# Performance work log

Measured on AMD Instinct MI355X. Metric: run time of the kernel, lower is better.

Reference implementation:

```python
import jax, jax.numpy as jnp
import numpy as np

EDGES_1B = [[1,2],[1,39],[2,3],[2,25],[3,4],[3,18],[4,5],[4,14],[5,6],[5,8],[6,7],[6,11],[7,8],[8,9],[9,39],[10,11],[10,13],[11,12],[13,14],[14,15],[15,16],[16,17],[16,19],[16,24],[17,18],[17,27],[19,20],[19,33],[20,21],[20,34],[21,22],[22,23],[22,35],[23,24],[23,36],[25,26],[25,37],[26,27],[26,28],[26,29],[28,29],[29,38],[30,38],[31,32],[33,34],[35,36]]
NUM_GRAPHS = 8192
NODES_PER_GRAPH = 39
HIDDEN = 128
NODE_F, EDGE_F, OUT_F = 4, 2, 2
EPS = 1e-5


def _build_edge_index():
    e0 = np.array([[u - 1, v - 1] for u, v in EDGES_1B], dtype=np.int64)
    e = np.concatenate([e0, e0[:, ::-1]], axis=0).T  # [2, 92] bidirectional
    off = np.arange(NUM_GRAPHS, dtype=np.int64) * NODES_PER_GRAPH
    ei = (e[:, None, :] + off[None, :, None]).reshape(2, -1)  # [2, 8192*92]
    return jnp.asarray(ei)


def setup_inputs() -> dict:
    key = jax.random.key(0)
    ks = jax.random.split(key, 16)
    N = NUM_GRAPHS * NODES_PER_GRAPH
    E = NUM_GRAPHS * 92

    def lin(k, fi, fo):
        k1, k2 = jax.random.split(k)
        s = 1.0 / np.sqrt(fi)
        return (jax.random.uniform(k1, (fi, fo), jnp.float32, -s, s),
                jax.random.uniform(k2, (fo,), jnp.float32, -s, s))

    W1a, b1a = lin(ks[0], 2 * NODE_F + EDGE_F, HIDDEN)
    W1b, b1b = lin(ks[1], HIDDEN, HIDDEN)
    W2a, b2a = lin(ks[2], 2 * HIDDEN + EDGE_F, HIDDEN)
    W2b, b2b = lin(ks[3], HIDDEN, HIDDEN)
    Wo, bo = lin(ks[4], HIDDEN, OUT_F)
    return {
        'x': jax.random.normal(ks[5], (N, NODE_F), jnp.float32),
        'edge_index': _build_edge_index(),
        'edge_attr': jax.random.normal(ks[6], (E, EDGE_F), jnp.float32),
        'W1a': W1a, 'b1a': b1a, 'W1b': W1b, 'b1b': b1b,
        'g1': jnp.ones((HIDDEN,), jnp.float32), 'be1': jnp.zeros((HIDDEN,), jnp.float32),
        'W2a': W2a, 'b2a': b2a, 'W2b': W2b, 'b2b': b2b,
        'g2': jnp.ones((HIDDEN,), jnp.float32), 'be2': jnp.zeros((HIDDEN,), jnp.float32),
        'Wo': Wo, 'bo': bo,
    }


def _gnn_layer(x, src, dst, edge_attr, Wa, ba, Wb, bb):
    # message: mlp(cat[x_i, x_j, edge_attr]) with x_i = target, x_j = source
    m = jnp.concatenate([x[dst], x[src], edge_attr], axis=1)  # [E, 2F+Fe]
    m = jax.nn.relu(m @ Wa + ba) @ Wb + bb                    # [E, H]
    N = x.shape[0]
    agg = jax.ops.segment_sum(m, dst, num_segments=N)         # scatter-sum
    cnt = jax.ops.segment_sum(jnp.ones((m.shape[0],), m.dtype), dst, num_segments=N)
    return agg / jnp.maximum(cnt, 1.0)[:, None]               # mean aggregation


def _batch_norm(x, gamma, beta):
    mu = jnp.mean(x, axis=0)
    var = jnp.mean(jnp.square(x - mu), axis=0)  # biased var (training-mode BN)
    return (x - mu) * jax.lax.rsqrt(var + EPS) * gamma + beta


def reference(x, edge_index, edge_attr, W1a, b1a, W1b, b1b, g1, be1,
              W2a, b2a, W2b, b2b, g2, be2, Wo, bo):
    src, dst = edge_index[0], edge_index[1]
    h = _gnn_layer(x, src, dst, edge_attr, W1a, b1a, W1b, b1b)
    h = jax.nn.relu(_batch_norm(h, g1, be1))
    h = _gnn_layer(h, src, dst, edge_attr, W2a, b2a, W2b, b2b)
    h = jax.nn.relu(_batch_norm(h, g2, be2))
    return h @ Wo + bo
```

## Files before the change

### kernel.cpp

```cpp
#include <hip/hip_runtime.h>
#include <hip/hip_bf16.h>

#define NG 8192
#define NPG 39
#define H 128
#define NTOT (NG*NPG)
#define INV_N (1.0f/319488.0f)
#define SHS 136

typedef __attribute__((ext_vector_type(8))) short bf16x8;
typedef __attribute__((ext_vector_type(4))) float f32x4;
typedef unsigned short u16;

__device__ __forceinline__ float u16tof(u16 u) {
  union { unsigned int i; float f; } v; v.i = ((unsigned int)u) << 16; return v.f;
}
__device__ __forceinline__ u16 ftou16(float f) {
  union { float f; unsigned int i; } v; v.f = f;
  const unsigned int x = v.i;
  return (u16)((x + 0x7FFFu + ((x >> 16) & 1u)) >> 16);
}

__constant__ int INC_OFF[40] = {0,2,5,8,11,14,17,19,22,24,26,29,30,32,35,37,41,44,46,49,
                                52,54,57,60,62,65,69,71,73,76,77,78,79,81,83,85,87,88,90,92};
__constant__ int INC_EID[92] = {
 46,47, 0,48,49, 2,50,51, 4,52,53, 6,54,55, 8,56,57, 10,58, 9,12,59, 13,60,
 61,62, 11,15,63, 17, 16,64, 7,18,65, 19,66, 20,67,68,69, 21,70,71, 5,24,
 22,72,73, 26,74,75, 28,76, 30,77,78, 31,79,80, 23,33, 3,81,82, 35,83,84,85,
 25,37, 38,86, 39,40,87, 88, 89, 43, 27,90, 29,44, 32,91, 34,45, 36, 41,42, 1,14};
__constant__ int INC_SRC[92] = {
 1,38, 0,2,24, 1,3,17, 2,4,13, 3,5,7, 4,6,10, 5,7, 4,6,8, 7,38,
 10,12, 5,9,11, 10, 9,13, 3,12,14, 13,15, 14,16,18,23, 15,17,26, 2,16,
 15,19,32, 18,20,33, 19,21, 20,22,34, 21,23,35, 15,22, 1,25,36, 24,26,27,28,
 16,25, 25,28, 25,27,37, 37, 31, 30, 18,33, 19,32, 21,35, 22,34, 24, 28,29, 0,8};
__constant__ float DEGINV[39] = {
 0.5f, 1.f/3, 1.f/3, 1.f/3, 1.f/3, 1.f/3, 0.5f, 1.f/3, 0.5f, 0.5f,
 1.f/3, 1.f,   0.5f, 1.f/3, 0.5f, 0.25f, 1.f/3, 0.5f, 1.f/3, 1.f/3,
 0.5f, 1.f/3, 1.f/3, 0.5f, 1.f/3, 0.25f, 0.5f, 0.5f, 1.f/3, 1.f,
 1.f,  1.f,   0.5f, 0.5f, 0.5f, 0.5f, 1.f,  0.5f, 0.5f};

__global__ __launch_bounds__(256)
void k_tr(const float* __restrict__ W2a, const float* __restrict__ W2b,
          const float* __restrict__ W1b, u16* __restrict__ WT)
{
  const int idx = blockIdx.x * 256 + threadIdx.x;
  const int mat = idx >> 14, rem = idx & 16383;
  const int n = rem >> 7, k = rem & 127;
  float v;
  if (mat == 0)      v = W2a[k*H + n];
  else if (mat == 1) v = W2a[(128 + k)*H + n];
  else if (mat == 2) v = W2b[k*H + n];
  else               v = W1b[k*H + n];
  WT[mat*16384 + n*128 + k] = ftou16(v);
}

__global__ __launch_bounds__(512, 8)
void k_layer1(const float* __restrict__ x, const float* __restrict__ ea,
              const float* __restrict__ W1a, const float* __restrict__ b1a,
              const u16* __restrict__ W1bT, const float* __restrict__ b1b,
              u16* __restrict__ h1, float* __restrict__ pstats)
{
  __shared__ alignas(16) u16 shb[48*SHS];
  __shared__ alignas(16) float sx[160];
  __shared__ alignas(16) float sea[184];
  const int g = blockIdx.x, tid = threadIdx.x;
  const int lane = tid & 63, wv = tid >> 6;
  const int qd = lane >> 4, ln = lane & 15;
  const int col = wv*16 + ln;

  for (int i = tid; i < 156; i += 512) sx[i] = x[g*156 + i];
  for (int i = tid; i < 184; i += 512) sea[i] = ea[g*184 + i];
  __syncthreads();

  {
    const int j = tid & 127;
    float wa[10];
    #pragma unroll
    for (int r = 0; r < 10; ++r) wa[r] = W1a[r*H + j];
    const float ba = b1a[j];
    for (int n = (tid >> 7); n < 39; n += 4) {
      const float4 xd = *(const float4*)&sx[n*4];
      const float xdot = ba + xd.x*wa[0] + xd.y*wa[1] + xd.z*wa[2] + xd.w*wa[3];
      float acc = 0.f;
      const int o1 = INC_OFF[n+1];
      for (int t = INC_OFF[n]; t < o1; ++t) {
        const int e = INC_EID[t], s = INC_SRC[t];
        const float4 xs = *(const float4*)&sx[s*4];
        const float2 se = *(const float2*)&sea[e*2];
        const float hv = xdot + xs.x*wa[4] + xs.y*wa[5] + xs.z*wa[6] + xs.w*wa[7]
                              + se.x*wa[8] + se.y*wa[9];
        acc += fmaxf(hv, 0.f);
      }
      shb[n*SHS + j] = ftou16(acc * DEGINV[n]);
    }
  }
  __syncthreads();

  {
    bf16x8 bw[4];
    const u16* wbp = W1bT + col*128 + qd*8;
    #pragma unroll
    for (int kt = 0; kt < 4; ++kt) bw[kt] = *(const bf16x8*)(wbp + kt*32);
    const float bcol = b1b[col];
    float ssum = 0.f, ssq = 0.f;
    #pragma unroll
    for (int mt = 0; mt < 3; ++mt) {
      bf16x8 a[4];
      const u16* ap = shb + (mt*16 + ln)*SHS + qd*8;
      #pragma unroll
      for (int kt = 0; kt < 4; ++kt) a[kt] = *(const bf16x8*)(ap + kt*32);
      f32x4 acc = {0.f,0.f,0.f,0.f};
      #pragma unroll
      for (int kt = 0; kt < 4; ++kt)
        acc = __builtin_amdgcn_mfma_f32_16x16x32_bf16(a[kt], bw[kt], acc, 0, 0, 0);
      #pragma unroll
      for (int r = 0; r < 4; ++r) {
        const int rw = mt*16 + qd*4 + r;
        if (rw < 39) {
          const float v = acc[r] + bcol;
          h1[(size_t)(g*39 + rw)*H + col] = ftou16(v);
          ssum += v; ssq += v*v;
        }
      }
    }
    ssum += __shfl_down(ssum, 32); ssum += __shfl_down(ssum, 16);
    ssq  += __shfl_down(ssq, 32);  ssq  += __shfl_down(ssq, 16);
    if (lane < 16) {
      pstats[(size_t)0*NG*H + (size_t)g*H + wv*16 + lane] = ssum;
      pstats[(size_t)1*NG*H + (size_t)g*H + wv*16 + lane] = ssq;
    }
  }
}

__global__ __launch_bounds__(256)
void k_red1(const float* __restrict__ pstats, float* __restrict__ part2)
{
  const int b = blockIdx.x, tid = threadIdx.x;
  const int j = tid & 127, p = tid >> 7;
  const float* base = pstats + (size_t)p*NG*H + (size_t)b*64*H + j;
  float s = 0.f;
  for (int r = 0; r < 64; ++r) s += base[r*H];
  part2[p*128*H + b*H + j] = s;
}

__global__ __launch_bounds__(256)
void k_red2(const float* __restrict__ part2, const float* __restrict__ gamma,
            const float* __restrict__ beta, float* __restrict__ sc)
{
  __shared__ float st[256];
  const int tid = threadIdx.x;
  const int j = tid & 127, p = tid >> 7;
  const float* base = part2 + p*128*H + j;
  float s = 0.f;
  for (int b = 0; b < 128; ++b) s += base[b*H];
  st[p*128 + j] = s;
  __syncthreads();
  if (tid < 128) {
    const float mu  = st[tid] * INV_N;
    const float var = st[128 + tid] * INV_N - mu*mu;
    const float inv = rsqrtf(fmaxf(var, 0.f) + 1e-5f);
    const float s1  = gamma[tid] * inv;
    sc[tid]       = s1;
    sc[128 + tid] = beta[tid] - mu * s1;
  }
}

__global__ __launch_bounds__(512, 8)
void k_layer2(const u16* __restrict__ h1, const float* __restrict__ ea,
              const float* __restrict__ sc1,
              const u16* __restrict__ WdT, const u16* __restrict__ WsT,
              const u16* __restrict__ WbT,
              const float* __restrict__ W2a, const float* __restrict__ b2a,
              const float* __restrict__ b2b,
              u16* __restrict__ h2, float* __restrict__ pstats)
{
  __shared__ alignas(16) u16 shb[48*SHS];
  __shared__ alignas(16) u16 pdb[48*SHS];
  __shared__ alignas(16) u16 psb[48*SHS];
  __shared__ alignas(16) float sea[184];
  const int g = blockIdx.x, tid = threadIdx.x;
  const int lane = tid & 63, wv = tid >> 6;
  const int qd = lane >> 4, ln = lane & 15;
  const int col = wv*16 + ln;

  for (int i = tid; i < 184; i += 512) sea[i] = ea[g*184 + i];
  {
    const u16* hp = h1 + (size_t)g*39*H;
    for (int i = tid; i < 1248; i += 512) {
      const int n = i >> 5, j = (i & 31) * 4;
      const ushort4 hv = ((const ushort4*)hp)[i];
      const float4 s0 = *(const float4*)&sc1[j];
      const float4 s1 = *(const float4*)&sc1[128 + j];
      ushort4 st;
      st.x = ftou16(fmaxf(u16tof(hv.x)*s0.x + s1.x, 0.f));
      st.y = ftou16(fmaxf(u16tof(hv.y)*s0.y + s1.y, 0.f));
      st.z = ftou16(fmaxf(u16tof(hv.z)*s0.z + s1.z, 0.f));
      st.w = ftou16(fmaxf(u16tof(hv.w)*s0.w + s1.w, 0.f));
      *(ushort4*)&shb[n*SHS + j] = st;
    }
  }
  __syncthreads();

  {
    bf16x8 bd[4], bs[4];
    const u16* wdp = WdT + col*128 + qd*8;
    const u16* wsp = WsT + col*128 + qd*8;
    #pragma unroll
    for (int kt = 0; kt < 4; ++kt) {
      bd[kt] = *(const bf16x8*)(wdp + kt*32);
      bs[kt] = *(const bf16x8*)(wsp + kt*32);
    }
    #pragma unroll
    for (int mt = 0; mt < 3; ++mt) {
      bf16x8 a[4];
      const u16* ap = shb + (mt*16 + ln)*SHS + qd*8;
      #pragma unroll
      for (int kt = 0; kt < 4; ++kt) a[kt] = *(const bf16x8*)(ap + kt*32);
      f32x4 accd = {0.f,0.f,0.f,0.f}, accs = {0.f,0.f,0.f,0.f};
      #pragma unroll
      for (int kt = 0; kt < 4; ++kt) {
        accd = __builtin_amdgcn_mfma_f32_16x16x32_bf16(a[kt], bd[kt], accd, 0, 0, 0);
        accs = __builtin_amdgcn_mfma_f32_16x16x32_bf16(a[kt], bs[kt], accs, 0, 0, 0);
      }
      #pragma unroll
      for (int r = 0; r < 4; ++r) {
        const int rw = mt*16 + qd*4 + r;
        pdb[rw*SHS + col] = ftou16(accd[r]);
        psb[rw*SHS + col] = ftou16(accs[r]);
      }
    }
  }
  __syncthreads();

  {
    const int j2 = tid & 63;
    const int nq = tid >> 6;
    const float2 w8 = *(const float2*)&W2a[256*H + 2*j2];
    const float2 w9 = *(const float2*)&W2a[257*H + 2*j2];
    const float2 b2 = *(const float2*)&b2a[2*j2];
    for (int n = nq; n < 39; n += 8) {
      const ushort2 pdu = *(const ushort2*)&pdb[n*SHS + 2*j2];
      const float base0 = u16tof(pdu.x) + b2.x;
      const float base1 = u16tof(pdu.y) + b2.y;
      float a0 = 0.f, a1 = 0.f;
      const int o1 = INC_OFF[n+1];
      for (int t = INC_OFF[n]; t < o1; ++t) {
        const int e = INC_EID[t], s = INC_SRC[t];
        const float2 se = *(const float2*)&sea[e*2];
        const ushort2 ps = *(const ushort2*)&psb[s*SHS + 2*j2];
        const float h0 = base0 + u16tof(ps.x) + se.x*w8.x + se.y*w9.x;
        const float h1v = base1 + u16tof(ps.y) + se.x*w8.y + se.y*w9.y;
        a0 += fmaxf(h0, 0.f);
        a1 += fmaxf(h1v, 0.f);
      }
      ushort2 st;
      st.x = ftou16(a0 * DEGINV[n]);
      st.y = ftou16(a1 * DEGINV[n]);
      *(ushort2*)&shb[n*SHS + 2*j2] = st;
    }
  }
  __syncthreads();

  {
    bf16x8 bb[4];
    const u16* wbp = WbT + col*128 + qd*8;
    #pragma unroll
    for (int kt = 0; kt < 4; ++kt) bb[kt] = *(const bf16x8*)(wbp + kt*32);
    const float bcol = b2b[col];
    float ssum = 0.f, ssq = 0.f;
    #pragma unroll
    for (int mt = 0; mt < 3; ++mt) {
      bf16x8 a[4];
      const u16* ap = shb + (mt*16 + ln)*SHS + qd*8;
      #pragma unroll
      for (int kt = 0; kt < 4; ++kt) a[kt] = *(const bf16x8*)(ap + kt*32);
      f32x4 acc = {0.f,0.f,0.f,0.f};
      #pragma unroll
      for (int kt = 0; kt < 4; ++kt)
        acc = __builtin_amdgcn_mfma_f32_16x16x32_bf16(a[kt], bb[kt], acc, 0, 0, 0);
      #pragma unroll
      for (int r = 0; r < 4; ++r) {
        const int rw = mt*16 + qd*4 + r;
        if (rw < 39) {
          const float v = acc[r] + bcol;
          h2[(size_t)(g*39 + rw)*H + col] = ftou16(v);
          ssum += v; ssq += v*v;
        }
      }
    }
    ssum += __shfl_down(ssum, 32); ssum += __shfl_down(ssum, 16);
    ssq  += __shfl_down(ssq, 32);  ssq  += __shfl_down(ssq, 16);
    if (lane < 16) {
      pstats[(size_t)0*NG*H + (size_t)g*H + wv*16 + lane] = ssum;
      pstats[(size_t)1*NG*H + (size_t)g*H + wv*16 + lane] = ssq;
    }
  }
}

__global__ __launch_bounds__(256)
void k_out(const u16* __restrict__ h2, const float* __restrict__ sc2,
           const float* __restrict__ Wo, const float* __restrict__ bo,
           float* __restrict__ out)
{
  const int tid = threadIdx.x;
  const int lane = tid & 63;
  const size_t n = (size_t)blockIdx.x*4 + (tid >> 6);
  const int c0 = lane, c1 = lane + 64;
  const float v0 = fmaxf(u16tof(h2[n*H + c0]) * sc2[c0] + sc2[128 + c0], 0.f);
  const float v1 = fmaxf(u16tof(h2[n*H + c1]) * sc2[c1] + sc2[128 + c1], 0.f);
  float a0 = v0*Wo[c0*2]   + v1*Wo[c1*2];
  float a1 = v0*Wo[c0*2+1] + v1*Wo[c1*2+1];
  #pragma unroll
  for (int off = 32; off > 0; off >>= 1) {
    a0 += __shfl_down(a0, off);
    a1 += __shfl_down(a1, off);
  }
  if (lane == 0) {
    *(float2*)&out[n*2] = make_float2(a0 + bo[0], a1 + bo[1]);
  }
}

extern "C" void kernel_launch(void* const* d_in, const int* in_sizes, int n_in,
                              void* d_out, int out_size, void* d_ws, size_t ws_size,
                              hipStream_t stream)
{
  const float* x   = (const float*)d_in[0];
  const float* ea  = (const float*)d_in[2];
  const float* W1a = (const float*)d_in[3];
  const float* b1a = (const float*)d_in[4];
  const float* W1b = (const float*)d_in[5];
  const float* b1b = (const float*)d_in[6];
  const float* g1  = (const float*)d_in[7];
  const float* be1 = (const float*)d_in[8];
  const float* W2a = (const float*)d_in[9];
  const float* b2a = (const float*)d_in[10];
  const float* W2b = (const float*)d_in[11];
  const float* b2b = (const float*)d_in[12];
  const float* g2  = (const float*)d_in[13];
  const float* be2 = (const float*)d_in[14];
  const float* Wo  = (const float*)d_in[15];
  const float* bo  = (const float*)d_in[16];
  float* out = (float*)d_out;

  char* ws = (char*)d_ws;
  size_t off = 0;
  u16* h1 = (u16*)(ws + off); off += (size_t)NTOT*H*2;
  u16* h2 = (u16*)(ws + off); off += (size_t)NTOT*H*2;
  float* pstats1 = (float*)(ws + off); off += (size_t)2*NG*H*4;
  float* pstats2 = (float*)(ws + off); off += (size_t)2*NG*H*4;
  float* p2a = (float*)(ws + off); off += (size_t)2*128*H*4;
  float* p2b = (float*)(ws + off); off += (size_t)2*128*H*4;
  float* sc1 = (float*)(ws + off); off += 256*4;
  float* sc2 = (float*)(ws + off); off += 256*4;
  u16* WT = (u16*)(ws + off); off += (size_t)4*16384*2;
  u16* WdT  = WT;
  u16* WsT  = WT + 16384;
  u16* WbT  = WT + 32768;
  u16* W1bT = WT + 49152;

  k_tr<<<256, 256, 0, stream>>>(W2a, W2b, W1b, WT);
  k_layer1<<<NG, 512, 0, stream>>>(x, ea, W1a, b1a, W1bT, b1b, h1, pstats1);
  k_red1<<<128, 256, 0, stream>>>(pstats1, p2a);
  k_red2<<<1, 256, 0, stream>>>(p2a, g1, be1, sc1);
  k_layer2<<<NG, 512, 0, stream>>>(h1, ea, sc1, WdT, WsT, WbT, W2a, b2a, b2b, h2, pstats2);
  k_red1<<<128, 256, 0, stream>>>(pstats2, p2b);
  k_red2<<<1, 256, 0, stream>>>(p2b, g2, be2, sc2);
  k_out<<<NTOT/4, 256, 0, stream>>>(h2, sc2, Wo, bo, out);
}
```

Measured before the change: 433.4 us.

## Compute layer-1 first edge MLP with bf16 MFMA over per-edge feature tiles

Layer 1's first linear layer was computed with scalar FMAs per (node, incident edge, hidden column). It now builds a padded bf16 edge-feature matrix [92 x 32] in shared memory, multiplies it by a pre-transposed bf16 W1a with one MFMA per 16-row tile, stores the ReLU'd messages in a new shared buffer, and then mean-aggregates them per node. This trades scalar ALU work for matrix-core work, but adds about 25 KB of shared memory per block, which may lower occupancy, and rounds the first-layer inputs and weights to bf16.

New measurement: 408.7 us. 5.7% less time.

```diff
diff --git a/kernel.cpp b/kernel.cpp
--- a/kernel.cpp
+++ b/kernel.cpp
@@ -7,8 +7,10 @@
 #define NTOT (NG*NPG)
 #define INV_N (1.0f/319488.0f)
 #define SHS 136
+#define ES 40
 
 typedef __attribute__((ext_vector_type(8))) short bf16x8;
+typedef __attribute__((ext_vector_type(8))) unsigned short u16x8;
 typedef __attribute__((ext_vector_type(4))) float f32x4;
 typedef unsigned short u16;
 
@@ -33,6 +35,12 @@
  10,12, 5,9,11, 10, 9,13, 3,12,14, 13,15, 14,16,18,23, 15,17,26, 2,16,
  15,19,32, 18,20,33, 19,21, 20,22,34, 21,23,35, 15,22, 1,25,36, 24,26,27,28,
  16,25, 25,28, 25,27,37, 37, 31, 30, 18,33, 19,32, 21,35, 22,34, 24, 28,29, 0,8};
+__constant__ int EDST[92] = {
+ 1,38,2,24,3,17,4,13,5,7,6,10,7,8,38,10,12,11,13,14,15,16,18,23,17,26,19,32,20,33,21,22,34,23,35,25,36,26,27,28,28,37,37,31,33,35,
+ 0,0,1,1,2,2,3,3,4,4,5,5,6,7,8,9,9,10,12,13,14,15,15,15,16,16,18,18,19,19,20,21,21,22,22,24,24,25,25,25,27,28,29,30,32,34};
+__constant__ int ESRC[92] = {
+ 0,0,1,1,2,2,3,3,4,4,5,5,6,7,8,9,9,10,12,13,14,15,15,15,16,16,18,18,19,19,20,21,21,22,22,24,24,25,25,25,27,28,29,30,32,34,
+ 1,38,2,24,3,17,4,13,5,7,6,10,7,8,38,10,12,11,13,14,15,16,18,23,17,26,19,32,20,33,21,22,34,23,35,25,36,26,27,28,28,37,37,31,33,35};
 __constant__ float DEGINV[39] = {
  0.5f, 1.f/3, 1.f/3, 1.f/3, 1.f/3, 1.f/3, 0.5f, 1.f/3, 0.5f, 0.5f,
  1.f/3, 1.f,   0.5f, 1.f/3, 0.5f, 0.25f, 1.f/3, 0.5f, 1.f/3, 1.f/3,
@@ -41,28 +49,38 @@
 
 __global__ __launch_bounds__(256)
 void k_tr(const float* __restrict__ W2a, const float* __restrict__ W2b,
-          const float* __restrict__ W1b, u16* __restrict__ WT)
+          const float* __restrict__ W1b, const float* __restrict__ W1a,
+          u16* __restrict__ WT)
 {
   const int idx = blockIdx.x * 256 + threadIdx.x;
-  const int mat = idx >> 14, rem = idx & 16383;
-  const int n = rem >> 7, k = rem & 127;
-  float v;
-  if (mat == 0)      v = W2a[k*H + n];
-  else if (mat == 1) v = W2a[(128 + k)*H + n];
-  else if (mat == 2) v = W2b[k*H + n];
-  else               v = W1b[k*H + n];
-  WT[mat*16384 + n*128 + k] = ftou16(v);
+  if (idx < 65536) {
+    const int mat = idx >> 14, rem = idx & 16383;
+    const int n = rem >> 7, k = rem & 127;
+    float v;
+    if (mat == 0)      v = W2a[k*H + n];
+    else if (mat == 1) v = W2a[(128 + k)*H + n];
+    else if (mat == 2) v = W2b[k*H + n];
+    else               v = W1b[k*H + n];
+    WT[mat*16384 + n*128 + k] = ftou16(v);
+  } else if (idx < 69632) {
+    const int rem = idx - 65536;
+    const int col = rem >> 5, k = rem & 31;
+    const float v = (k < 10) ? W1a[k*H + col] : 0.f;
+    WT[65536 + col*32 + k] = ftou16(v);
+  }
 }
 
 __global__ __launch_bounds__(512, 8)
 void k_layer1(const float* __restrict__ x, const float* __restrict__ ea,
-              const float* __restrict__ W1a, const float* __restrict__ b1a,
+              const u16* __restrict__ W1aT, const float* __restrict__ b1a,
               const u16* __restrict__ W1bT, const float* __restrict__ b1b,
               u16* __restrict__ h1, float* __restrict__ pstats)
 {
   __shared__ alignas(16) u16 shb[48*SHS];
+  __shared__ alignas(16) u16 msgb[92*SHS];
   __shared__ alignas(16) float sx[160];
   __shared__ alignas(16) float sea[184];
+  u16* Eb = shb;
   const int g = blockIdx.x, tid = threadIdx.x;
   const int lane = tid & 63, wv = tid >> 6;
   const int qd = lane >> 4, ln = lane & 15;
@@ -72,26 +90,58 @@
   for (int i = tid; i < 184; i += 512) sea[i] = ea[g*184 + i];
   __syncthreads();
 
-  {
-    const int j = tid & 127;
-    float wa[10];
-    #pragma unroll
-    for (int r = 0; r < 10; ++r) wa[r] = W1a[r*H + j];
-    const float ba = b1a[j];
-    for (int n = (tid >> 7); n < 39; n += 4) {
-      const float4 xd = *(const float4*)&sx[n*4];
-      const float xdot = ba + xd.x*wa[0] + xd.y*wa[1] + xd.z*wa[2] + xd.w*wa[3];
-      float acc = 0.f;
+  if (tid < 92) {
+    const int e = tid;
+    const int d = EDST[e], s = ESRC[e];
+    u16x8 r0, r1, z;
+    r0[0] = ftou16(sx[d*4]);   r0[1] = ftou16(sx[d*4+1]);
+    r0[2] = ftou16(sx[d*4+2]); r0[3] = ftou16(sx[d*4+3]);
+    r0[4] = ftou16(sx[s*4]);   r0[5] = ftou16(sx[s*4+1]);
+    r0[6] = ftou16(sx[s*4+2]); r0[7] = ftou16(sx[s*4+3]);
+    r1[0] = ftou16(sea[e*2]);  r1[1] = ftou16(sea[e*2+1]);
+    #pragma unroll
+    for (int q = 2; q < 8; ++q) r1[q] = 0;
+    #pragma unroll
+    for (int q = 0; q < 8; ++q) z[q] = 0;
+    *(u16x8*)&Eb[e*ES]      = r0;
+    *(u16x8*)&Eb[e*ES + 8]  = r1;
+    *(u16x8*)&Eb[e*ES + 16] = z;
+    *(u16x8*)&Eb[e*ES + 24] = z;
+  }
+  __syncthreads();
+
+  {
+    const bf16x8 bw = *(const bf16x8*)(W1aT + col*32 + qd*8);
+    const float bcol = b1a[col];
+    #pragma unroll
+    for (int mt = 0; mt < 6; ++mt) {
+      const bf16x8 a = *(const bf16x8*)&Eb[(mt*16 + ln)*ES + qd*8];
+      f32x4 acc = {0.f,0.f,0.f,0.f};
+      acc = __builtin_amdgcn_mfma_f32_16x16x32_bf16(a, bw, acc, 0, 0, 0);
+      #pragma unroll
+      for (int r = 0; r < 4; ++r) {
+        const int rw = mt*16 + qd*4 + r;
+        if (rw < 92) msgb[rw*SHS + col] = ftou16(fmaxf(acc[r] + bcol, 0.f));
+      }
+    }
+  }
+  __syncthreads();
+
+  {
+    const int j2 = tid & 63;
+    const int nq = tid >> 6;
+    for (int n = nq; n < 39; n += 8) {
+      float a0 = 0.f, a1 = 0.f;
       const int o1 = INC_OFF[n+1];
       for (int t = INC_OFF[n]; t < o1; ++t) {
-        const int e = INC_EID[t], s = INC_SRC[t];
-        const float4 xs = *(const float4*)&sx[s*4];
-        const float2 se = *(const float2*)&sea[e*2];
-        const float hv = xdot + xs.x*wa[4] + xs.y*wa[5] + xs.z*wa[6] + xs.w*wa[7]
-                              + se.x*wa[8] + se.y*wa[9];
-        acc += fmaxf(hv, 0.f);
-      }
-      shb[n*SHS + j] = ftou16(acc * DEGINV[n]);
+        const int e = INC_EID[t];
+        const ushort2 m = *(const ushort2*)&msgb[e*SHS + 2*j2];
+        a0 += u16tof(m.x); a1 += u16tof(m.y);
+      }
+      ushort2 st;
+      st.x = ftou16(a0 * DEGINV[n]);
+      st.y = ftou16(a1 * DEGINV[n]);
+      *(ushort2*)&shb[n*SHS + 2*j2] = st;
     }
   }
   __syncthreads();
@@ -352,14 +402,15 @@
   float* p2b = (float*)(ws + off); off += (size_t)2*128*H*4;
   float* sc1 = (float*)(ws + off); off += 256*4;
   float* sc2 = (float*)(ws + off); off += 256*4;
-  u16* WT = (u16*)(ws + off); off += (size_t)4*16384*2;
+  u16* WT = (u16*)(ws + off); off += (size_t)(4*16384 + 4096)*2;
   u16* WdT  = WT;
   u16* WsT  = WT + 16384;
   u16* WbT  = WT + 32768;
   u16* W1bT = WT + 49152;
-
-  k_tr<<<256, 256, 0, stream>>>(W2a, W2b, W1b, WT);
-  k_layer1<<<NG, 512, 0, stream>>>(x, ea, W1a, b1a, W1bT, b1b, h1, pstats1);
+  u16* W1aT = WT + 65536;
+
+  k_tr<<<272, 256, 0, stream>>>(W2a, W2b, W1b, W1a, WT);
+  k_layer1<<<NG, 512, 0, stream>>>(x, ea, W1aT, b1a, W1bT, b1b, h1, pstats1);
   k_red1<<<128, 256, 0, stream>>>(pstats1, p2a);
   k_red2<<<1, 256, 0, stream>>>(p2a, g1, be1, sc1);
   k_layer2<<<NG, 512, 0, stream>>>(h1, ea, sc1, WdT, WsT, WbT, W2a, b2a, b2b, h2, pstats2);
```
